# Kernel optimization log

Measured on AMD Instinct MI355X. Metric: run time of the kernel, lower is better.

## Reference

```python
import jax, jax.numpy as jnp
import numpy as np
from functools import partial

N_USERS = 100000
N_ITEMS = 50000
EMB = 64
N_FACTORS = 4
N_ITER = 2
N_LAYERS = 2
E = 2000000
EPS = 1e-12  # F.normalize eps


def setup_inputs() -> dict:
    key = jax.random.key(0)
    k1, k2, k3, k4 = jax.random.split(key, 4)
    N = N_USERS + N_ITEMS
    user_emb = jax.random.normal(k1, (N_USERS, EMB), jnp.float32) * 0.1
    item_emb = jax.random.normal(k2, (N_ITEMS, EMB), jnp.float32) * 0.1
    # first N entries cover every node once so row/col degree sums are > 0
    # (original norm_adj has no isolated nodes; avoids 1/sqrt(0))
    h = jnp.concatenate([jnp.arange(N, dtype=jnp.int32),
                         jax.random.randint(k3, (E - N,), 0, N, jnp.int32)])
    t = jnp.concatenate([jnp.arange(N, dtype=jnp.int32)[::-1],
                         jax.random.randint(k4, (E - N,), 0, N, jnp.int32)])
    return {"user_emb": user_emb, "item_emb": item_emb, "h_list": h, "t_list": t}


def _l2norm(x):
    n = jnp.sqrt(jnp.sum(x * x, axis=-1, keepdims=True))
    return x / jnp.maximum(n, EPS)


def _dgcf_embed(user_emb, item_emb, h_list, t_list):
    N = user_emb.shape[0] + item_emb.shape[0]
    d = user_emb.shape[1]
    F = N_FACTORS
    df = d // F
    Ee = h_list.shape[0]
    seg = partial(jax.ops.segment_sum, num_segments=N)
    seg_h = jax.vmap(lambda v: seg(v, h_list))  # batched over factor axis

    ego = jnp.concatenate([user_emb, item_emb], 0)  # [N, d]
    all_embeds = [ego]
    A_values = jnp.ones((F, Ee), ego.dtype)  # routing logits, persist across layers

    for _ in range(N_LAYERS):
        x = ego.reshape(N, F, df).transpose(1, 0, 2)  # [F, N, df] factor chunks
        out = x
        for _ in range(N_ITER):
            scores = jax.nn.softmax(A_values, axis=0)        # [F, E]
            rowsum = seg_h(scores)                           # [F, N] sparse.sum(A, dim=1)
            d_col = 1.0 / jnp.sqrt(rowsum)                   # [F, N]
            # out = D_col @ A @ D_col @ x  (original uses D_col on both sides)
            y = d_col[:, :, None] * x                        # [F, N, df]
            msg = scores[:, :, None] * y[:, t_list, :]       # [F, E, df]
            out = d_col[:, :, None] * seg_h(msg)             # [F, N, df]
            # routing score update: cosine-ish affinity head(new) vs tanh(tail(old))
            head = _l2norm(out[:, h_list, :])                # [F, E, df]
            tail = _l2norm(x[:, t_list, :])                  # [F, E, df]
            A_values = A_values + jnp.sum(head * jnp.tanh(tail), axis=-1)
        ego = out.transpose(1, 0, 2).reshape(N, d)           # concat factor outputs
        all_embeds.append(ego)

    all_emb = jnp.mean(jnp.stack(all_embeds, 1), axis=1)     # [N, d]
    return all_emb[:user_emb.shape[0]], all_emb[user_emb.shape[0]:]


def reference(user_emb, item_emb, h_list, t_list):
    return _dgcf_embed(user_emb, item_emb, h_list, t_list)
```

## Files before the change

### kernel.cpp

```cpp
#include <hip/hip_runtime.h>
#include <hip/hip_bf16.h>

#define DEMB 64
typedef unsigned short u16;
typedef float f32x2 __attribute__((ext_vector_type(2)));

__device__ __forceinline__ u16 f2bf(float f) {
    union { float f; unsigned int i; } c; c.f = f;
    unsigned int r = c.i + 0x7FFF + ((c.i >> 16) & 1);
    return (u16)(r >> 16);
}
__device__ __forceinline__ float lo16(unsigned int w) {
    union { unsigned int i; float f; } c; c.i = w << 16; return c.f;
}
__device__ __forceinline__ float hi16(unsigned int w) {
    union { unsigned int i; float f; } c; c.i = w & 0xFFFF0000u; return c.f;
}

__device__ __forceinline__ float ptanh5(float a) {
    float a2 = a * a;
    float t = fmaf(a2, -0.030095f, 0.124066f);
    t = fmaf(a2, t, -0.332377f);
    t = fmaf(a2, t, 1.0f);
    return a * t;
}

__global__ void init_A_kernel(float4* __restrict__ A, int E) {
    int e = blockIdx.x * blockDim.x + threadIdx.x;
    if (e < E) A[e] = make_float4(1.f, 1.f, 1.f, 1.f);
}

__global__ void concat_copy_kernel(const float* __restrict__ u, const float* __restrict__ it,
                                   float* __restrict__ x, float* __restrict__ acc,
                                   int nu_elems, int total) {
    int i = blockIdx.x * blockDim.x + threadIdx.x;
    if (i >= total) return;
    float v = (i < nu_elems) ? u[i] : it[i - nu_elems];
    x[i] = v;
    acc[i] = v;
}

__global__ void hist_kernel(const int* __restrict__ h, int* __restrict__ ghist,
                            int E, int EPB, int NB) {
    __shared__ int bins[1024];
    int b = blockIdx.x, tid = threadIdx.x;
    for (int j = tid; j < NB; j += 256) bins[j] = 0;
    __syncthreads();
    int s = b * EPB, e = min(s + EPB, E);
    for (int k = s + tid; k < e; k += 256)
        atomicAdd(&bins[((unsigned)h[k]) >> 8], 1);
    __syncthreads();
    for (int j = tid; j < NB; j += 256) ghist[j * gridDim.x + b] = bins[j];
}

__global__ void btot_kernel(const int* __restrict__ ghist, int* __restrict__ btot) {
    __shared__ int s[256];
    int j = blockIdx.x, tid = threadIdx.x;
    s[tid] = ghist[j * 256 + tid];
    __syncthreads();
    for (int o = 128; o >= 1; o >>= 1) {
        if (tid < o) s[tid] += s[tid + o];
        __syncthreads();
    }
    if (tid == 0) btot[j] = s[0];
}

__global__ void bscan_kernel(const int* __restrict__ btot, int* __restrict__ bbase,
                             int NB, int E) {
    __shared__ int s[1024];
    int tid = threadIdx.x;
    int v = (tid < NB) ? btot[tid] : 0;
    s[tid] = v;
    __syncthreads();
    for (int o = 1; o < 1024; o <<= 1) {
        int a = (tid >= o) ? s[tid - o] : 0;
        __syncthreads();
        s[tid] += a;
        __syncthreads();
    }
    if (tid < NB) bbase[tid] = s[tid] - v;
    if (tid == 0) bbase[NB] = E;
}

__global__ void bofs_kernel(int* __restrict__ ghist, const int* __restrict__ bbase) {
    __shared__ int s[256];
    int j = blockIdx.x, tid = threadIdx.x;
    int v = ghist[j * 256 + tid];
    s[tid] = v;
    __syncthreads();
    for (int o = 1; o < 256; o <<= 1) {
        int a = (tid >= o) ? s[tid - o] : 0;
        __syncthreads();
        s[tid] += a;
        __syncthreads();
    }
    ghist[j * 256 + tid] = bbase[j] + s[tid] - v;
}

__global__ void scatter_kernel(const int* __restrict__ h, const int* __restrict__ t,
                               const int* __restrict__ ghist, unsigned* __restrict__ stg,
                               int E, int EPB, int NB) {
    __shared__ int cur[1024];
    int b = blockIdx.x, tid = threadIdx.x;
    for (int j = tid; j < NB; j += 256) cur[j] = ghist[j * gridDim.x + b];
    __syncthreads();
    int s = b * EPB, e = min(s + EPB, E);
    for (int k = s + tid; k < e; k += 256) {
        unsigned hh = (unsigned)h[k];
        int pos = atomicAdd(&cur[hh >> 8], 1);
        stg[pos] = ((hh & 255u) << 18) | (unsigned)t[k];
    }
}

__global__ void finalize_kernel(const unsigned* __restrict__ stg, const int* __restrict__ bbase,
                                int* __restrict__ off, int* __restrict__ csr_t, int N, int E) {
    __shared__ int cnt[256];
    __shared__ int scn[256];
    int b = blockIdx.x, tid = threadIdx.x;
    int ebeg = bbase[b], eend = bbase[b + 1];
    cnt[tid] = 0;
    __syncthreads();
    for (int k = ebeg + tid; k < eend; k += 256)
        atomicAdd(&cnt[(stg[k] >> 18) & 255u], 1);
    __syncthreads();
    int v = cnt[tid];
    scn[tid] = v;
    __syncthreads();
    for (int o = 1; o < 256; o <<= 1) {
        int a = (tid >= o) ? scn[tid - o] : 0;
        __syncthreads();
        scn[tid] += a;
        __syncthreads();
    }
    int excl = scn[tid] - v;
    int gn = (b << 8) + tid;
    if (gn < N) off[gn] = ebeg + excl;
    if (b == 0 && tid == 0) off[N] = E;
    __syncthreads();
    cnt[tid] = excl;
    __syncthreads();
    for (int k = ebeg + tid; k < eend; k += 256) {
        unsigned en = stg[k];
        int slot = atomicAdd(&cnt[(en >> 18) & 255u], 1);
        csr_t[ebeg + slot] = (int)(en & 0x3FFFFu);
    }
}

__global__ void dcol0_kernel(const int* __restrict__ off, float* __restrict__ dcol, int N) {
    int n = blockIdx.x * blockDim.x + threadIdx.x;
    if (n >= N) return;
    float v = 0.5f * rsqrtf((float)(off[n + 1] - off[n]));
    *(float4*)(dcol + (size_t)n * 4) = make_float4(v, v, v, v);
}

__global__ void prep_kernel(const float* __restrict__ x, u16* __restrict__ xs,
                            u16* __restrict__ tailt, int total) {
    int i = blockIdx.x * blockDim.x + threadIdx.x;
    if (i >= total) return;
    float v = x[i];
    xs[i] = f2bf(v);
    float s = v * v;
#pragma unroll
    for (int o = 8; o >= 1; o >>= 1) s += __shfl_xor(s, o);
    float nr = fmaxf(sqrtf(s), 1e-12f);
    tailt[i] = f2bf(ptanh5(v * __builtin_amdgcn_rcpf(nr)));
}

template <bool UNI, bool WOUT, bool ROUTE, int ACC>
__global__ void message_kernel(const int* __restrict__ off, const int* __restrict__ csr_t,
                               float* __restrict__ Acsr, float* __restrict__ prob,
                               const u16* __restrict__ xs, const u16* __restrict__ tailt,
                               const float* __restrict__ dcol_in, float* __restrict__ dcol_out,
                               float* __restrict__ out, float* __restrict__ acc, int N) {
    int gid = blockIdx.x * blockDim.x + threadIdx.x;
    int n = gid >> 6;
    if (n >= N) return;
    int l = gid & 63;
    int g = l >> 4;
    int m = l & 15;
    unsigned f = (unsigned)(m >> 2);
    int s = off[n], e = off[n + 1];
    unsigned moff = (unsigned)(m << 2);

    f32x2 a01 = {0.f, 0.f}, a23 = {0.f, 0.f};

#pragma unroll 2
    for (int k = s; k < e; k += 8) {
        int e1 = k + g, e2 = e1 + 4;
        bool v1 = e1 < e, v2 = e2 < e;
        unsigned c1 = (unsigned)(v1 ? e1 : s);
        unsigned c2 = (unsigned)(v2 ? e2 : s);
        unsigned t1 = (unsigned)csr_t[c1];
        unsigned t2 = (unsigned)csr_t[c2];
        float p1, p2;
        if (UNI) {
            p1 = dcol_in[t1 * 4u + f];
            p2 = dcol_in[t2 * 4u + f];
        } else {
            p1 = prob[c1 * 4u + f] * dcol_in[t1 * 4u + f];
            p2 = prob[c2 * 4u + f] * dcol_in[t2 * 4u + f];
        }
        p1 = v1 ? p1 : 0.f;
        p2 = v2 ? p2 : 0.f;
        const uint2 x1 = *(const uint2*)(xs + (t1 << 6) + moff);
        const uint2 x2 = *(const uint2*)(xs + (t2 << 6) + moff);
        f32x2 xa = {lo16(x1.x), hi16(x1.x)};
        f32x2 xb = {lo16(x1.y), hi16(x1.y)};
        f32x2 ya = {lo16(x2.x), hi16(x2.x)};
        f32x2 yb = {lo16(x2.y), hi16(x2.y)};
        a01 += p1 * xa + p2 * ya;
        a23 += p1 * xb + p2 * yb;
    }

    float a0 = a01.x, a1 = a01.y, a2 = a23.x, a3 = a23.y;
    a0 += __shfl_xor(a0, 16); a1 += __shfl_xor(a1, 16);
    a2 += __shfl_xor(a2, 16); a3 += __shfl_xor(a3, 16);
    a0 += __shfl_xor(a0, 32); a1 += __shfl_xor(a1, 32);
    a2 += __shfl_xor(a2, 32); a3 += __shfl_xor(a3, 32);

    if (WOUT || ACC != 0) {
        float dn = dcol_in[(unsigned)n * 4u + f];
        if (l < 16) {
            unsigned oidx = ((unsigned)n << 6) + moff;
            float4 val = make_float4(a0 * dn, a1 * dn, a2 * dn, a3 * dn);
            if (WOUT) *(float4*)(out + oidx) = val;
            if (ACC == 1) {
                float4 c = *(const float4*)(acc + oidx);
                *(float4*)(acc + oidx) =
                    make_float4(c.x + val.x, c.y + val.y, c.z + val.z, c.w + val.w);
            } else if (ACC == 2) {
                const float k3 = 1.0f / 3.0f;
                float4 c = *(const float4*)(acc + oidx);
                *(float4*)(acc + oidx) =
                    make_float4((c.x + val.x) * k3, (c.y + val.y) * k3,
                                (c.z + val.z) * k3, (c.w + val.w) * k3);
            }
        }
    }
    if (!ROUTE) return;

    float ss = a0 * a0 + a1 * a1 + a2 * a2 + a3 * a3;
    ss += __shfl_xor(ss, 1);
    ss += __shfl_xor(ss, 2);
    float inv = 1.0f / fmaxf(sqrtf(ss), 1e-12f);
    f32x2 h01 = {a0 * inv, a1 * inv};
    f32x2 h23 = {a2 * inv, a3 * inv};

    float rowsumf = 0.f;

#pragma unroll 2
    for (int k = s; k < e; k += 8) {
        int e1 = k + g, e2 = e1 + 4;
        bool v1 = e1 < e, v2 = e2 < e;
        unsigned c1 = (unsigned)(v1 ? e1 : s);
        unsigned c2 = (unsigned)(v2 ? e2 : s);
        unsigned t1 = (unsigned)csr_t[c1];
        unsigned t2 = (unsigned)csr_t[c2];
        const uint2 tv1 = *(const uint2*)(tailt + (t1 << 6) + moff);
        const uint2 tv2 = *(const uint2*)(tailt + (t2 << 6) + moff);
        f32x2 dv1 = h01 * (f32x2){lo16(tv1.x), hi16(tv1.x)}
                  + h23 * (f32x2){lo16(tv1.y), hi16(tv1.y)};
        f32x2 dv2 = h01 * (f32x2){lo16(tv2.x), hi16(tv2.x)}
                  + h23 * (f32x2){lo16(tv2.y), hi16(tv2.y)};
        float d1 = dv1.x + dv1.y;
        float d2 = dv2.x + dv2.y;
        d1 += __shfl_xor(d1, 1); d1 += __shfl_xor(d1, 2);
        d2 += __shfl_xor(d2, 1); d2 += __shfl_xor(d2, 2);
        unsigned ai1 = c1 * 4u + f;
        unsigned ai2 = c2 * 4u + f;
        float na1 = Acsr[ai1] + d1;
        float na2 = Acsr[ai2] + d2;
        float ex1 = __expf(na1);
        float ex2 = __expf(na2);
        float se1 = ex1 + __shfl_xor(ex1, 4); se1 += __shfl_xor(se1, 8);
        float se2 = ex2 + __shfl_xor(ex2, 4); se2 += __shfl_xor(se2, 8);
        float p1 = ex1 * __builtin_amdgcn_rcpf(se1);
        float p2 = ex2 * __builtin_amdgcn_rcpf(se2);
        if ((m & 3) == 0) {
            if (v1) { Acsr[ai1] = na1; prob[ai1] = p1; }
            if (v2) { Acsr[ai2] = na2; prob[ai2] = p2; }
        }
        rowsumf += (v1 ? p1 : 0.f) + (v2 ? p2 : 0.f);
    }

    rowsumf += __shfl_xor(rowsumf, 16);
    rowsumf += __shfl_xor(rowsumf, 32);
    if (l < 16 && (m & 3) == 0) dcol_out[(unsigned)n * 4u + f] = rsqrtf(rowsumf);
}

extern "C" void kernel_launch(void* const* d_in, const int* in_sizes, int n_in,
                              void* d_out, int out_size, void* d_ws, size_t ws_size,
                              hipStream_t stream) {
    const float* user_emb = (const float*)d_in[0];
    const float* item_emb = (const float*)d_in[1];
    const int* h = (const int*)d_in[2];
    const int* t = (const int*)d_in[3];

    const int nu_elems = in_sizes[0];
    const int ni_elems = in_sizes[1];
    const int total = nu_elems + ni_elems;
    const int N = total / DEMB;
    const int E = in_sizes[2];
    const int NB = (N + 255) >> 8;
    const int NBLK = 256;
    const int EPB = (E + NBLK - 1) / NBLK;

    float* acc = (float*)d_out;

    float* x     = (float*)d_ws;
    float* out   = x + (size_t)total;
    float* Acsr  = out + (size_t)total;
    float* prob  = Acsr + (size_t)4 * E;
    float* dcolA = prob + (size_t)4 * E;
    float* dcolB = dcolA + (size_t)4 * N;
    u16* xs      = (u16*)(dcolB + (size_t)4 * N);
    u16* tailt   = xs + (size_t)total;
    int* ghist   = (int*)(tailt + (size_t)total);
    int* btot    = ghist + (size_t)NB * 256;
    int* bbase   = btot + ((NB + 3) & ~3);
    int* off     = bbase + ((NB + 5) & ~3);
    int* csr_t   = off + ((N + 4) & ~3);
    unsigned* stg = (unsigned*)prob;

    const int BLK = 256;
    const int gE = (E + BLK - 1) / BLK;
    const int gTot = (total + BLK - 1) / BLK;
    const int gN = (N + BLK - 1) / BLK;
    const int gNodeWave = (N * 64 + BLK - 1) / BLK;

    concat_copy_kernel<<<gTot, BLK, 0, stream>>>(user_emb, item_emb, x, acc, nu_elems, total);

    hist_kernel<<<NBLK, 256, 0, stream>>>(h, ghist, E, EPB, NB);
    btot_kernel<<<NB, 256, 0, stream>>>(ghist, btot);
    bscan_kernel<<<1, 1024, 0, stream>>>(btot, bbase, NB, E);
    bofs_kernel<<<NB, 256, 0, stream>>>(ghist, bbase);
    scatter_kernel<<<NBLK, 256, 0, stream>>>(h, t, ghist, stg, E, EPB, NB);
    finalize_kernel<<<NB, 256, 0, stream>>>(stg, bbase, off, csr_t, N, E);

    init_A_kernel<<<gE, BLK, 0, stream>>>((float4*)Acsr, E);
    dcol0_kernel<<<gN, BLK, 0, stream>>>(off, dcolA, N);

    prep_kernel<<<gTot, BLK, 0, stream>>>(x, xs, tailt, total);
    message_kernel<true, false, true, 0><<<gNodeWave, BLK, 0, stream>>>(
        off, csr_t, Acsr, prob, xs, tailt, dcolA, dcolB, out, acc, N);
    message_kernel<false, true, true, 1><<<gNodeWave, BLK, 0, stream>>>(
        off, csr_t, Acsr, prob, xs, tailt, dcolB, dcolA, out, acc, N);

    prep_kernel<<<gTot, BLK, 0, stream>>>(out, xs, tailt, total);
    message_kernel<false, false, true, 0><<<gNodeWave, BLK, 0, stream>>>(
        off, csr_t, Acsr, prob, xs, tailt, dcolA, dcolB, x, acc, N);
    message_kernel<false, false, false, 2><<<gNodeWave, BLK, 0, stream>>>(
        off, csr_t, Acsr, prob, xs, tailt, dcolB, dcolA, x, acc, N);
}
```

Measured before the change: 590.1 us.

## Interleave bf16 x and tanh-tail into one array and reuse gathered rows in routing

The prep kernel now packs the bf16 embedding and the bf16 tanh-normalized tail into a single 32-bit word per element. The message kernel gathers 16 bytes per neighbor chunk, which carries both values at once. It processes the first 16 edges of each node unconditionally and keeps their gathered words in registers, so the routing pass reuses them instead of reloading csr_t and the tail rows. The inner loops now step over 4 edges per iteration instead of 8. The cost is that low-degree nodes still issue masked loads for all 16 slots, and the final non-routing kernel reads tail data it never uses.

```diff
diff --git a/kernel.cpp b/kernel.cpp
--- a/kernel.cpp
+++ b/kernel.cpp
@@ -5,10 +5,10 @@
 typedef unsigned short u16;
 typedef float f32x2 __attribute__((ext_vector_type(2)));
 
-__device__ __forceinline__ u16 f2bf(float f) {
+__device__ __forceinline__ unsigned f2bf(float f) {
     union { float f; unsigned int i; } c; c.f = f;
     unsigned int r = c.i + 0x7FFF + ((c.i >> 16) & 1);
-    return (u16)(r >> 16);
+    return r >> 16;
 }
 __device__ __forceinline__ float lo16(unsigned int w) {
     union { unsigned int i; float f; } c; c.i = w << 16; return c.f;
@@ -153,23 +153,22 @@
     *(float4*)(dcol + (size_t)n * 4) = make_float4(v, v, v, v);
 }
 
-__global__ void prep_kernel(const float* __restrict__ x, u16* __restrict__ xs,
-                            u16* __restrict__ tailt, int total) {
+__global__ void prep_kernel(const float* __restrict__ x, unsigned* __restrict__ xt, int total) {
     int i = blockIdx.x * blockDim.x + threadIdx.x;
     if (i >= total) return;
     float v = x[i];
-    xs[i] = f2bf(v);
     float s = v * v;
 #pragma unroll
     for (int o = 8; o >= 1; o >>= 1) s += __shfl_xor(s, o);
     float nr = fmaxf(sqrtf(s), 1e-12f);
-    tailt[i] = f2bf(ptanh5(v * __builtin_amdgcn_rcpf(nr)));
+    unsigned tb = f2bf(ptanh5(v * __builtin_amdgcn_rcpf(nr)));
+    xt[i] = (tb << 16) | f2bf(v);
 }
 
 template <bool UNI, bool WOUT, bool ROUTE, int ACC>
 __global__ void message_kernel(const int* __restrict__ off, const int* __restrict__ csr_t,
                                float* __restrict__ Acsr, float* __restrict__ prob,
-                               const u16* __restrict__ xs, const u16* __restrict__ tailt,
+                               const unsigned* __restrict__ xt,
                                const float* __restrict__ dcol_in, float* __restrict__ dcol_out,
                                float* __restrict__ out, float* __restrict__ acc, int N) {
     int gid = blockIdx.x * blockDim.x + threadIdx.x;
@@ -184,32 +183,29 @@
 
     f32x2 a01 = {0.f, 0.f}, a23 = {0.f, 0.f};
 
+    auto trip = [&](int kbase, uint4& w) {
+        int e1 = kbase + g;
+        bool v1 = e1 < e;
+        unsigned c1 = (unsigned)(v1 ? e1 : s);
+        unsigned t1 = (unsigned)csr_t[c1];
+        float p1;
+        if (UNI) p1 = dcol_in[t1 * 4u + f];
+        else     p1 = prob[c1 * 4u + f] * dcol_in[t1 * 4u + f];
+        p1 = v1 ? p1 : 0.f;
+        w = *(const uint4*)(xt + (t1 << 6) + moff);
+        a01 += p1 * (f32x2){lo16(w.x), lo16(w.y)};
+        a23 += p1 * (f32x2){lo16(w.z), lo16(w.w)};
+    };
+
+    uint4 w0, w1, w2, w3;
+    trip(s, w0);
+    trip(s + 4, w1);
+    trip(s + 8, w2);
+    trip(s + 12, w3);
 #pragma unroll 2
-    for (int k = s; k < e; k += 8) {
-        int e1 = k + g, e2 = e1 + 4;
-        bool v1 = e1 < e, v2 = e2 < e;
-        unsigned c1 = (unsigned)(v1 ? e1 : s);
-        unsigned c2 = (unsigned)(v2 ? e2 : s);
-        unsigned t1 = (unsigned)csr_t[c1];
-        unsigned t2 = (unsigned)csr_t[c2];
-        float p1, p2;
-        if (UNI) {
-            p1 = dcol_in[t1 * 4u + f];
-            p2 = dcol_in[t2 * 4u + f];
-        } else {
-            p1 = prob[c1 * 4u + f] * dcol_in[t1 * 4u + f];
-            p2 = prob[c2 * 4u + f] * dcol_in[t2 * 4u + f];
-        }
-        p1 = v1 ? p1 : 0.f;
-        p2 = v2 ? p2 : 0.f;
-        const uint2 x1 = *(const uint2*)(xs + (t1 << 6) + moff);
-        const uint2 x2 = *(const uint2*)(xs + (t2 << 6) + moff);
-        f32x2 xa = {lo16(x1.x), hi16(x1.x)};
-        f32x2 xb = {lo16(x1.y), hi16(x1.y)};
-        f32x2 ya = {lo16(x2.x), hi16(x2.x)};
-        f32x2 yb = {lo16(x2.y), hi16(x2.y)};
-        a01 += p1 * xa + p2 * ya;
-        a23 += p1 * xb + p2 * yb;
+    for (int k = s + 16; k < e; k += 4) {
+        uint4 wt;
+        trip(k, wt);
     }
 
     float a0 = a01.x, a1 = a01.y, a2 = a23.x, a3 = a23.y;
@@ -248,39 +244,34 @@
 
     float rowsumf = 0.f;
 
+    auto route = [&](int kbase, const uint4& w) {
+        int e1 = kbase + g;
+        bool v1 = e1 < e;
+        unsigned c1 = (unsigned)(v1 ? e1 : s);
+        f32x2 dv = h01 * (f32x2){hi16(w.x), hi16(w.y)}
+                 + h23 * (f32x2){hi16(w.z), hi16(w.w)};
+        float d1 = dv.x + dv.y;
+        d1 += __shfl_xor(d1, 1); d1 += __shfl_xor(d1, 2);
+        unsigned ai = c1 * 4u + f;
+        float na = Acsr[ai] + d1;
+        float ex = __expf(na);
+        float se = ex + __shfl_xor(ex, 4); se += __shfl_xor(se, 8);
+        float p = ex * __builtin_amdgcn_rcpf(se);
+        if ((m & 3) == 0 && v1) { Acsr[ai] = na; prob[ai] = p; }
+        rowsumf += v1 ? p : 0.f;
+    };
+
+    route(s, w0);
+    route(s + 4, w1);
+    route(s + 8, w2);
+    route(s + 12, w3);
 #pragma unroll 2
-    for (int k = s; k < e; k += 8) {
-        int e1 = k + g, e2 = e1 + 4;
-        bool v1 = e1 < e, v2 = e2 < e;
-        unsigned c1 = (unsigned)(v1 ? e1 : s);
-        unsigned c2 = (unsigned)(v2 ? e2 : s);
+    for (int k = s + 16; k < e; k += 4) {
+        int e1 = k + g;
+        unsigned c1 = (unsigned)((e1 < e) ? e1 : s);
         unsigned t1 = (unsigned)csr_t[c1];
-        unsigned t2 = (unsigned)csr_t[c2];
-        const uint2 tv1 = *(const uint2*)(tailt + (t1 << 6) + moff);
-        const uint2 tv2 = *(const uint2*)(tailt + (t2 << 6) + moff);
-        f32x2 dv1 = h01 * (f32x2){lo16(tv1.x), hi16(tv1.x)}
-                  + h23 * (f32x2){lo16(tv1.y), hi16(tv1.y)};
-        f32x2 dv2 = h01 * (f32x2){lo16(tv2.x), hi16(tv2.x)}
-                  + h23 * (f32x2){lo16(tv2.y), hi16(tv2.y)};
-        float d1 = dv1.x + dv1.y;
-        float d2 = dv2.x + dv2.y;
-        d1 += __shfl_xor(d1, 1); d1 += __shfl_xor(d1, 2);
-        d2 += __shfl_xor(d2, 1); d2 += __shfl_xor(d2, 2);
-        unsigned ai1 = c1 * 4u + f;
-        unsigned ai2 = c2 * 4u + f;
-        float na1 = Acsr[ai1] + d1;
-        float na2 = Acsr[ai2] + d2;
-        float ex1 = __expf(na1);
-        float ex2 = __expf(na2);
-        float se1 = ex1 + __shfl_xor(ex1, 4); se1 += __shfl_xor(se1, 8);
-        float se2 = ex2 + __shfl_xor(ex2, 4); se2 += __shfl_xor(se2, 8);
-        float p1 = ex1 * __builtin_amdgcn_rcpf(se1);
-        float p2 = ex2 * __builtin_amdgcn_rcpf(se2);
-        if ((m & 3) == 0) {
-            if (v1) { Acsr[ai1] = na1; prob[ai1] = p1; }
-            if (v2) { Acsr[ai2] = na2; prob[ai2] = p2; }
-        }
-        rowsumf += (v1 ? p1 : 0.f) + (v2 ? p2 : 0.f);
+        uint4 wt = *(const uint4*)(xt + (t1 << 6) + moff);
+        route(k, wt);
     }
 
     rowsumf += __shfl_xor(rowsumf, 16);
@@ -313,9 +304,8 @@
     float* prob  = Acsr + (size_t)4 * E;
     float* dcolA = prob + (size_t)4 * E;
     float* dcolB = dcolA + (size_t)4 * N;
-    u16* xs      = (u16*)(dcolB + (size_t)4 * N);
-    u16* tailt   = xs + (size_t)total;
-    int* ghist   = (int*)(tailt + (size_t)total);
+    unsigned* xt = (unsigned*)(dcolB + (size_t)4 * N);
+    int* ghist   = (int*)(xt + (size_t)total);
     int* btot    = ghist + (size_t)NB * 256;
     int* bbase   = btot + ((NB + 3) & ~3);
     int* off     = bbase + ((NB + 5) & ~3);
@@ -340,15 +330,15 @@
     init_A_kernel<<<gE, BLK, 0, stream>>>((float4*)Acsr, E);
     dcol0_kernel<<<gN, BLK, 0, stream>>>(off, dcolA, N);
 
-    prep_kernel<<<gTot, BLK, 0, stream>>>(x, xs, tailt, total);
+    prep_kernel<<<gTot, BLK, 0, stream>>>(x, xt, total);
     message_kernel<true, false, true, 0><<<gNodeWave, BLK, 0, stream>>>(
-        off, csr_t, Acsr, prob, xs, tailt, dcolA, dcolB, out, acc, N);
+        off, csr_t, Acsr, prob, xt, dcolA, dcolB, out, acc, N);
     message_kernel<false, true, true, 1><<<gNodeWave, BLK, 0, stream>>>(
-        off, csr_t, Acsr, prob, xs, tailt, dcolB, dcolA, out, acc, N);
-
-    prep_kernel<<<gTot, BLK, 0, stream>>>(out, xs, tailt, total);
+        off, csr_t, Acsr, prob, xt, dcolB, dcolA, out, acc, N);
+
+    prep_kernel<<<gTot, BLK, 0, stream>>>(out, xt, total);
     message_kernel<false, false, true, 0><<<gNodeWave, BLK, 0, stream>>>(
-        off, csr_t, Acsr, prob, xs, tailt, dcolA, dcolB, x, acc, N);
+        off, csr_t, Acsr, prob, xt, dcolA, dcolB, x, acc, N);
     message_kernel<false, false, false, 2><<<gNodeWave, BLK, 0, stream>>>(
-        off, csr_t, Acsr, prob, xs, tailt, dcolB, dcolA, x, acc, N);
-}
+        off, csr_t, Acsr, prob, xt, dcolB, dcolA, x, acc, N);
+}
```

New measurement: 610.9 us. +3.5%, slower.
